# Performance work log

Hardware: AMD Instinct MI355X
Metric: run time of the kernel (lower is better)

## Reference

```python
import jax, jax.numpy as jnp
import numpy as np

B, C, H, W = 8, 256, 32, 32
DK, HEADS = 64, 4
DQ = DK * HEADS            # lambda attention: query dim = dim_key * num_heads
DV = 256 // HEADS          # out_channels // num_heads
EPS = 1e-5
SF = DK ** (-0.25)


def setup_inputs() -> dict:
    key = jax.random.key(0)
    ks = jax.random.split(key, 6)
    inv = 1.0 / np.sqrt(C)
    return {
        "input": jax.random.normal(ks[0], (B, C, H, W), jnp.float32),
        "Wq": jax.random.normal(ks[1], (DQ, C), jnp.float32) * inv,
        "gamma_q": jnp.ones((DQ,), jnp.float32),
        "beta_q": jnp.zeros((DQ,), jnp.float32),
        "Wk": jax.random.normal(ks[2], (DK, C), jnp.float32) * inv,
        "gamma_k": jnp.ones((DK,), jnp.float32),
        "beta_k": jnp.zeros((DK,), jnp.float32),
        "Wv": jax.random.normal(ks[3], (DV, C), jnp.float32) * inv,
        "rpe": jax.random.normal(ks[4], (2 * max(H, W) - 1, 2 * max(H, W) - 1, DK), jnp.float32),
    }


def _bn(x, gamma, beta):
    # BatchNorm2d in training mode: batch stats over (B, H, W), biased variance
    mu = jnp.mean(x, axis=(0, 2, 3), keepdims=True)
    var = jnp.var(x, axis=(0, 2, 3), keepdims=True)
    xn = (x - mu) * jax.lax.rsqrt(var + EPS)
    return xn * gamma[None, :, None, None] + beta[None, :, None, None]


def reference(input, Wq, gamma_q, beta_q, Wk, gamma_k, beta_k, Wv, rpe):
    b, c, h, w = input.shape
    n = h * w
    size = max(h, w)

    # conv1x1 projections (no bias)
    q = _bn(jnp.einsum('oc,bchw->bohw', Wq, input), gamma_q, beta_q)
    k = _bn(jnp.einsum('oc,bchw->bohw', Wk, input), gamma_k, beta_k)
    v = jnp.einsum('oc,bchw->bohw', Wv, input)

    q = q.reshape(b, HEADS, DK, n) * SF          # [b,h,k,n]
    k = k.reshape(b, DK, n) * SF                 # single kv head -> [b,k,n]
    v = v.reshape(b, DV, n)                      # [b,v,n]

    # lambda attention: content lambda
    ks = jax.nn.softmax(k, axis=-1)
    context = jnp.einsum('bkn,bvn->bkv', ks, v)
    out = jnp.einsum('bkv,bhkn->bhvn', context, q)

    # positional lambda via relative position embedding gather
    pos = jnp.arange(size)
    grid = jnp.stack(jnp.meshgrid(pos, pos, indexing='ij'), axis=-1).reshape(-1, 2)  # [n,2]
    rel = grid[None, :] - grid[:, None] + (size - 1)                                 # [n,n,2]
    rg = rpe[rel[..., 0], rel[..., 1]]                                               # [n,n,k]
    pos_context = jnp.einsum('nmk,bvm->bnkv', rg, v)
    out = out + jnp.einsum('bhkn,bnkv->bhvn', q, pos_context)

    return out.reshape(b, -1, h, w)
```

## Files before the change

### kernel.cpp

```cpp
#include <hip/hip_runtime.h>

#define SFC 0.35355339059327373f

typedef __attribute__((ext_vector_type(8))) short short8;
typedef __attribute__((ext_vector_type(16))) float f32x16;
typedef unsigned short ushort_t;

__device__ __forceinline__ float4 ld4(const float* p) { return *reinterpret_cast<const float4*>(p); }
__device__ __forceinline__ void st4(float* p, float4 v) { *reinterpret_cast<float4*>(p) = v; }

union F4 { float4 v; float f[4]; };
union S8 { short8 v; ushort_t u[8]; };

__device__ __forceinline__ ushort_t bfb(float f) {
  union { float f; unsigned u; } a; a.f = f;
  unsigned r = a.u + 0x7FFFu + ((a.u >> 16) & 1u);
  return (ushort_t)(r >> 16);
}

__device__ __forceinline__ void gl16(const void* g, void* l) {
  __builtin_amdgcn_global_load_lds(
      (const __attribute__((address_space(1))) unsigned int*)g,
      (__attribute__((address_space(3))) unsigned int*)l, 16, 0, 0);
}

__global__ __launch_bounds__(256) void k_prep(
    const float* __restrict__ rpe, const float* __restrict__ wq,
    const float* __restrict__ wk, const float* __restrict__ wv,
    const float* __restrict__ x, ushort_t* __restrict__ RPEB,
    ushort_t* __restrict__ WB, ushort_t* __restrict__ XBT)
{
  const int bx = blockIdx.x, t = threadIdx.x;
  if (bx < 63) {
    const int di = bx;
#pragma unroll
    for (int i = 0; i < 2; ++i) {
      const int c = t + i * 256;
      if (c < 504) {
        const int dj = c >> 3, k8 = (c & 7) * 8;
        const float* s = rpe + (size_t)di * 4032 + dj * 64 + k8;
        float4 a = ld4(s), b = ld4(s + 4);
        S8 o;
        o.u[0] = bfb(a.x); o.u[1] = bfb(a.y); o.u[2] = bfb(a.z); o.u[3] = bfb(a.w);
        o.u[4] = bfb(b.x); o.u[5] = bfb(b.y); o.u[6] = bfb(b.z); o.u[7] = bfb(b.w);
        *(short8*)(RPEB + (size_t)di * 4608 + dj * 72 + k8) = o.v;
      }
    }
  } else if (bx < 111) {
    const int cc = (bx - 63) * 256 + t;
    const int o = cc >> 5, k8 = (cc & 31) * 8;
    const float* src = (o < 256) ? (wq + o * 256)
                      : (o < 320) ? (wk + (o - 256) * 256)
                                  : (wv + (o - 320) * 256);
    float4 a = ld4(src + k8), b = ld4(src + k8 + 4);
    S8 s;
    s.u[0] = bfb(a.x); s.u[1] = bfb(a.y); s.u[2] = bfb(a.z); s.u[3] = bfb(a.w);
    s.u[4] = bfb(b.x); s.u[5] = bfb(b.y); s.u[6] = bfb(b.z); s.u[7] = bfb(b.w);
    *(short8*)(WB + (size_t)o * 256 + k8) = s.v;
  } else {
    const int id = (bx - 111) * 256 + t;
    const int ng = id & 8191, c8 = id >> 13;
    const int bb = ng >> 10, nn = ng & 1023;
    const float* src = x + (size_t)bb * 262144 + (size_t)(c8 * 8) * 1024 + nn;
    S8 s;
#pragma unroll
    for (int j = 0; j < 8; ++j) s.u[j] = bfb(src[(size_t)j * 1024]);
    *(short8*)(XBT + (size_t)ng * 256 + c8 * 8) = s.v;
  }
}

__global__ __launch_bounds__(256) void k_projm(
    const ushort_t* __restrict__ WB, const ushort_t* __restrict__ XBT,
    float* __restrict__ P, ushort_t* __restrict__ VB)
{
  __shared__ ushort_t At[64 * 72];
  __shared__ ushort_t Bt[128 * 72];
  const int t = threadIdx.x;
  const int bm = blockIdx.x, bn = blockIdx.y;
  const int o0 = bm * 64, col0 = bn * 128;
  const int w = t >> 6, l = t & 63, ln = l & 31, hi = l >> 5;
  const int wm = w & 1, wn = w >> 1;

  f32x16 acc0, acc1;
#pragma unroll
  for (int i = 0; i < 16; ++i) { acc0[i] = 0.f; acc1[i] = 0.f; }

  for (int k0 = 0; k0 < 256; k0 += 64) {
    __syncthreads();
#pragma unroll
    for (int i = 0; i < 2; ++i) {
      const int c = t + i * 256, row = c >> 3, k8 = (c & 7) * 8;
      *(short8*)(At + row * 72 + k8) =
          *(const short8*)(WB + (size_t)(o0 + row) * 256 + k0 + k8);
    }
#pragma unroll
    for (int i = 0; i < 4; ++i) {
      const int c = t + i * 256, row = c >> 3, k8 = (c & 7) * 8;
      *(short8*)(Bt + row * 72 + k8) =
          *(const short8*)(XBT + (size_t)(col0 + row) * 256 + k0 + k8);
    }
    __syncthreads();
    const ushort_t* ka  = At + (wm * 32 + ln) * 72 + hi * 8;
    const ushort_t* kb0 = Bt + (wn * 64 + ln) * 72 + hi * 8;
    const ushort_t* kb1 = Bt + (wn * 64 + 32 + ln) * 72 + hi * 8;
#pragma unroll
    for (int kc = 0; kc < 4; ++kc) {
      short8 a = *(const short8*)(ka + kc * 16);
      acc0 = __builtin_amdgcn_mfma_f32_32x32x16_bf16(a, *(const short8*)(kb0 + kc * 16), acc0, 0, 0, 0);
      acc1 = __builtin_amdgcn_mfma_f32_32x32x16_bf16(a, *(const short8*)(kb1 + kc * 16), acc1, 0, 0, 0);
    }
  }

#pragma unroll
  for (int r = 0; r < 16; ++r) {
    const int o = o0 + wm * 32 + (r & 3) + 8 * (r >> 2) + 4 * hi;
    float* dst = P + (size_t)o * 8192 + col0 + wn * 64 + ln;
    dst[0]  = acc0[r];
    dst[32] = acc1[r];
  }
  if (bm == 5) {
    const int b2 = bn >> 3;
#pragma unroll
    for (int r = 0; r < 16; ++r) {
      const int v = wm * 32 + (r & 3) + 8 * (r >> 2) + 4 * hi;
      const int i20 = (bn & 7) * 4 + wn * 2;
      VB[(size_t)(b2 * 32 + i20) * 2560 + v * 40 + ln]     = bfb(acc0[r]);
      VB[(size_t)(b2 * 32 + i20 + 1) * 2560 + v * 40 + ln] = bfb(acc1[r]);
    }
  }
}

__global__ __launch_bounds__(256) void k_stats(
    const float* __restrict__ P, const float* __restrict__ gq,
    const float* __restrict__ bq, const float* __restrict__ gk,
    const float* __restrict__ bk, float* __restrict__ scale,
    float* __restrict__ shift)
{
  const int ch = blockIdx.x;
  const float4* row = (const float4*)(P + (size_t)ch * 8192);
  float s = 0.f, ss = 0.f;
  for (int i = threadIdx.x; i < 2048; i += 256) {
    float4 v = row[i];
    s  += v.x + v.y + v.z + v.w;
    ss += v.x * v.x + v.y * v.y + v.z * v.z + v.w * v.w;
  }
#pragma unroll
  for (int off = 32; off; off >>= 1) {
    s  += __shfl_down(s, off, 64);
    ss += __shfl_down(ss, off, 64);
  }
  __shared__ float red[8];
  const int w = threadIdx.x >> 6, lane = threadIdx.x & 63;
  if (lane == 0) { red[w] = s; red[4 + w] = ss; }
  __syncthreads();
  if (threadIdx.x == 0) {
    s = red[0] + red[1] + red[2] + red[3];
    ss = red[4] + red[5] + red[6] + red[7];
    const float mu = s * (1.0f / 8192.0f);
    const float var = ss * (1.0f / 8192.0f) - mu * mu;
    const float rsig = rsqrtf(var + 1e-5f);
    float g, be;
    if (ch < 256) { g = gq[ch]; be = bq[ch]; }
    else          { g = gk[ch - 256]; be = bk[ch - 256]; }
    const float sc = rsig * g * SFC;
    scale[ch] = sc;
    shift[ch] = be * SFC - mu * sc;
  }
}

__global__ __launch_bounds__(256) void k_softmax(
    const float* __restrict__ P, const float* __restrict__ scale,
    const float* __restrict__ shift, float* __restrict__ KS)
{
  const int b = blockIdx.x >> 6, kc = blockIdx.x & 63;
  const int ch = 256 + kc;
  const float4* row = (const float4*)(P + (size_t)ch * 8192 + b * 1024);
  const float sc = scale[ch], sh = shift[ch];
  float4 v = row[threadIdx.x];
  float y0 = v.x * sc + sh, y1 = v.y * sc + sh;
  float y2 = v.z * sc + sh, y3 = v.w * sc + sh;
  float m = fmaxf(fmaxf(y0, y1), fmaxf(y2, y3));
#pragma unroll
  for (int off = 32; off; off >>= 1) m = fmaxf(m, __shfl_xor(m, off, 64));
  __shared__ float red[8];
  const int w = threadIdx.x >> 6, lane = threadIdx.x & 63;
  if (lane == 0) red[w] = m;
  __syncthreads();
  m = fmaxf(fmaxf(red[0], red[1]), fmaxf(red[2], red[3]));
  const float e0 = __expf(y0 - m), e1 = __expf(y1 - m);
  const float e2 = __expf(y2 - m), e3 = __expf(y3 - m);
  float su = e0 + e1 + e2 + e3;
#pragma unroll
  for (int off = 32; off; off >>= 1) su += __shfl_xor(su, off, 64);
  if (lane == 0) red[4 + w] = su;
  __syncthreads();
  const float inv = 1.0f / (red[4] + red[5] + red[6] + red[7]);
  ((float4*)(KS + (size_t)(b * 64 + kc) * 1024))[threadIdx.x] =
      make_float4(e0 * inv, e1 * inv, e2 * inv, e3 * inv);
}

__global__ __launch_bounds__(256) void k_ctx(
    const float* __restrict__ KS, const float* __restrict__ P,
    float* __restrict__ ctxp)
{
  __shared__ float ksl[64][64];
  __shared__ float vl[64][64];
  const int t = threadIdx.x;
  const int b = blockIdx.x;
  const int n0 = blockIdx.y * 64;
  {
    const int c = t >> 2, q4 = (t & 3) * 16;
    const float* s = KS + (size_t)(b * 64 + c) * 1024 + n0 + q4;
#pragma unroll
    for (int i = 0; i < 16; ++i) ksl[q4 + i][c] = s[i];
    const float* v = P + (size_t)(320 + c) * 8192 + b * 1024 + n0 + q4;
#pragma unroll
    for (int i = 0; i < 16; ++i) vl[q4 + i][c] = v[i];
  }
  __syncthreads();
  const int tr = t >> 4, tc = t & 15;
  float acc[4][4] = {};
#pragma unroll 4
  for (int nn = 0; nn < 64; ++nn) {
    F4 a; a.v = ld4(&ksl[nn][tr * 4]);
    F4 bv; bv.v = ld4(&vl[nn][tc * 4]);
#pragma unroll
    for (int i = 0; i < 4; ++i)
#pragma unroll
      for (int j = 0; j < 4; ++j) acc[i][j] += a.f[i] * bv.f[j];
  }
  float* dst = ctxp + (size_t)(b * 16 + blockIdx.y) * 4096;
#pragma unroll
  for (int i = 0; i < 4; ++i)
    st4(dst + (tr * 4 + i) * 64 + tc * 4,
        make_float4(acc[i][0], acc[i][1], acc[i][2], acc[i][3]));
}

__global__ __launch_bounds__(256) void k_ctxred(
    const float* __restrict__ ctxp, ushort_t* __restrict__ ctxb)
{
  const int i = blockIdx.x * 256 + threadIdx.x;
  const int b = i >> 12, r = i & 4095, kc = r >> 6, vc = r & 63;
  float s = 0.f;
#pragma unroll
  for (int c = 0; c < 16; ++c) s += ctxp[(size_t)(b * 16 + c) * 4096 + r];
  ctxb[(size_t)b * 4608 + vc * 72 + kc] = bfb(s);
}

extern __shared__ char ldsc[];

__global__ __launch_bounds__(512) void k_pos(
    const float* __restrict__ P, const ushort_t* __restrict__ RPEB,
    const ushort_t* __restrict__ VB, const float* __restrict__ scale,
    const float* __restrict__ shift, const ushort_t* __restrict__ CTXB,
    float* __restrict__ out)
{
  float* qst = (float*)ldsc;
  char* RbC = ldsc + 33792;
  char* VbC = ldsc + 70656;
  ushort_t* SlB = (ushort_t*)(ldsc + 91136);

  const int t = threadIdx.x;
  const int b = blockIdx.x >> 5, i1 = blockIdx.x & 31;
  const int w = t >> 6, l = t & 63, ln = l & 31, hi = l >> 5;
  const int m = w & 3, g = w >> 2;

  auto stage = [&](int i2, int buf) {
    const char* rs = (const char*)RPEB + (size_t)(i2 - i1 + 31) * 9216;
    const char* vs = (const char*)VB + (size_t)(b * 32 + i2) * 5120;
    char* rd = RbC + g * 18432 + buf * 9216;
    char* vd = VbC + g * 10240 + buf * 5120;
#pragma unroll
    for (int j = 0; j < 4; ++j) {
      const int chunk = m * 4 + j;
      const int off = chunk * 1024 + l * 16;
      if (chunk < 9)       gl16(rs + off, rd + off);
      else if (chunk < 14) gl16(vs + off - 9216, vd + off - 9216);
    }
  };

  const int i2base = g * 16;
  stage(i2base, 0);

  {
    const int j1 = t & 31, c0 = (t >> 5) * 16;
    const float* src = P + (size_t)b * 1024 + i1 * 32 + j1;
#pragma unroll
    for (int i = 0; i < 16; ++i) {
      const int ch = c0 + i;
      qst[ch * 33 + j1] = src[(size_t)ch * 8192] * scale[ch] + shift[ch];
    }
  }
  __syncthreads();

  short8 qf[4];
#pragma unroll
  for (int kc = 0; kc < 4; ++kc) {
    S8 s;
#pragma unroll
    for (int i = 0; i < 8; ++i)
      s.u[i] = bfb(qst[(m * 64 + kc * 16 + hi * 8 + i) * 33 + ln]);
    qf[kc] = s.v;
  }

  f32x16 sv0, sv1;
#pragma unroll
  for (int i = 0; i < 16; ++i) { sv0[i] = 0.f; sv1[i] = 0.f; }

  ushort_t* sm = SlB + w * 1280;

  for (int s = 0; s < 16; ++s) {
    const int cur = s & 1;
    if (s + 1 < 16) stage(i2base + s + 1, cur ^ 1);

    f32x16 t0, t1;
#pragma unroll
    for (int i = 0; i < 16; ++i) { t0[i] = 0.f; t1[i] = 0.f; }
    {
      const ushort_t* rb = (const ushort_t*)(RbC + g * 18432 + cur * 9216);
      const ushort_t* r0 = rb + ln * 72 + hi * 8;
      const ushort_t* r1 = rb + (32 + ln) * 72 + hi * 8;
#pragma unroll
      for (int kc = 0; kc < 4; ++kc) {
        t0 = __builtin_amdgcn_mfma_f32_32x32x16_bf16(qf[kc], *(const short8*)(r0 + kc * 16), t0, 0, 0, 0);
        t1 = __builtin_amdgcn_mfma_f32_32x32x16_bf16(qf[kc], *(const short8*)(r1 + kc * 16), t1, 0, 0, 0);
      }
    }
#pragma unroll
    for (int r = 0; r < 16; ++r) {
      const int j1 = (r & 3) + 8 * (r >> 2) + 4 * hi;
      const int j2a = ln + j1 - 31;
      const int j2b = 32 + ln + j1 - 31;
      if ((unsigned)j2a < 32u) sm[j1 * 40 + j2a] = bfb(t0[r]);
      if ((unsigned)j2b < 32u) sm[j1 * 40 + j2b] = bfb(t1[r]);
    }
    {
      const ushort_t* sa = sm + ln * 40 + hi * 8;
      const ushort_t* vbp = (const ushort_t*)(VbC + g * 10240 + cur * 5120);
      const ushort_t* v0 = vbp + ln * 40 + hi * 8;
      const ushort_t* v1 = vbp + (32 + ln) * 40 + hi * 8;
      short8 sA0 = *(const short8*)(sa);
      short8 sA1 = *(const short8*)(sa + 16);
      sv0 = __builtin_amdgcn_mfma_f32_32x32x16_bf16(sA0, *(const short8*)(v0),      sv0, 0, 0, 0);
      sv0 = __builtin_amdgcn_mfma_f32_32x32x16_bf16(sA1, *(const short8*)(v0 + 16), sv0, 0, 0, 0);
      sv1 = __builtin_amdgcn_mfma_f32_32x32x16_bf16(sA0, *(const short8*)(v1),      sv1, 0, 0, 0);
      sv1 = __builtin_amdgcn_mfma_f32_32x32x16_bf16(sA1, *(const short8*)(v1 + 16), sv1, 0, 0, 0);
    }
    __syncthreads();
  }

  {
    const char* cs = (const char*)CTXB + (size_t)b * 9216;
    gl16(cs + w * 1024 + l * 16, RbC + w * 1024 + l * 16);
    if (w == 0) gl16(cs + 8192 + l * 16, RbC + 8192 + l * 16);
  }
  __syncthreads();

  float* out_l = qst;
  if (g == 0) {
    const ushort_t* cb = (const ushort_t*)RbC;
    const ushort_t* c0 = cb + ln * 72 + hi * 8;
    const ushort_t* c1 = cb + (32 + ln) * 72 + hi * 8;
#pragma unroll
    for (int kc = 0; kc < 4; ++kc) {
      sv0 = __builtin_amdgcn_mfma_f32_32x32x16_bf16(qf[kc], *(const short8*)(c0 + kc * 16), sv0, 0, 0, 0);
      sv1 = __builtin_amdgcn_mfma_f32_32x32x16_bf16(qf[kc], *(const short8*)(c1 + kc * 16), sv1, 0, 0, 0);
    }
  } else {
#pragma unroll
    for (int r = 0; r < 16; ++r) {
      const int j1 = (r & 3) + 8 * (r >> 2) + 4 * hi;
      out_l[(m * 64 + ln) * 33 + j1]      = sv0[r];
      out_l[(m * 64 + 32 + ln) * 33 + j1] = sv1[r];
    }
  }
  __syncthreads();
  if (g == 0) {
#pragma unroll
    for (int r = 0; r < 16; ++r) {
      const int j1 = (r & 3) + 8 * (r >> 2) + 4 * hi;
      out_l[(m * 64 + ln) * 33 + j1]      += sv0[r];
      out_l[(m * 64 + 32 + ln) * 33 + j1] += sv1[r];
    }
  }
  __syncthreads();
  {
    const int ch = t >> 1, jh = (t & 1) * 16;
    float* dst = out + (size_t)b * 262144 + (size_t)ch * 1024 + i1 * 32 + jh;
    const float* srow = out_l + ch * 33 + jh;
#pragma unroll
    for (int gq2 = 0; gq2 < 4; ++gq2)
      st4(dst + gq2 * 4, make_float4(srow[gq2 * 4], srow[gq2 * 4 + 1],
                                     srow[gq2 * 4 + 2], srow[gq2 * 4 + 3]));
  }
}

extern "C" void kernel_launch(void* const* d_in, const int* in_sizes, int n_in,
                              void* d_out, int out_size, void* d_ws, size_t ws_size,
                              hipStream_t stream) {
  const float* x   = (const float*)d_in[0];
  const float* wq  = (const float*)d_in[1];
  const float* gq  = (const float*)d_in[2];
  const float* bq  = (const float*)d_in[3];
  const float* wk  = (const float*)d_in[4];
  const float* gk  = (const float*)d_in[5];
  const float* bk  = (const float*)d_in[6];
  const float* wv  = (const float*)d_in[7];
  const float* rpe = (const float*)d_in[8];
  float* out = (float*)d_out;
  char* W = (char*)d_ws;

  float* P        = (float*)W;
  float* KS       = (float*)(W + 12582912);
  float* SCALE    = (float*)(W + 14680064);
  float* SHIFT    = (float*)(W + 14681344);
  float* CTXP     = (float*)(W + 14682624);
  ushort_t* CTXB  = (ushort_t*)(W + 16779776);
  ushort_t* RPEB  = (ushort_t*)(W + 16853504);
  ushort_t* VB    = (ushort_t*)(W + 17434112);
  ushort_t* WB    = (ushort_t*)(W + 18744832);
  ushort_t* XBT   = (ushort_t*)(W + 18941440);

  k_prep<<<1135, 256, 0, stream>>>(rpe, wq, wk, wv, x, RPEB, WB, XBT);
  k_projm<<<dim3(6, 64), 256, 0, stream>>>(WB, XBT, P, VB);
  k_stats<<<320, 256, 0, stream>>>(P, gq, bq, gk, bk, SCALE, SHIFT);
  k_softmax<<<512, 256, 0, stream>>>(P, SCALE, SHIFT, KS);
  k_ctx<<<dim3(8, 16), 256, 0, stream>>>(KS, P, CTXP);
  k_ctxred<<<128, 256, 0, stream>>>(CTXP, CTXB);

  hipFuncSetAttribute((const void*)k_pos,
                      hipFuncAttributeMaxDynamicSharedMemorySize, 111616);
  k_pos<<<256, 512, 111616, stream>>>(P, RPEB, VB, SCALE, SHIFT, CTXB, out);
}
```

Baseline: 64.69 us.

## Fuse BN stats into projection GEMM, MFMA context kernel, deeper k_pos pipeline

The separate BatchNorm stats pass is removed. The projection GEMM epilogue now reduces per-channel sum and sum-of-squares with shuffles and atomics, and consumers compute scale and shift inline. The context reduction is rewritten as a single bf16 MFMA kernel over all n, with softmax writing bf16, which replaces the fp32 partial-sum kernel and its separate reduction. k_pos moves from double buffering to a 4-slot buffer ring with prefetch distance 2, explicit vmcnt waits and setprio around the MFMAs. The cost is more LDS, float atomic nondeterminism, and k_ctxm running only 8 blocks.

```diff
diff --git a/kernel.cpp b/kernel.cpp
--- a/kernel.cpp
+++ b/kernel.cpp
@@ -28,11 +28,15 @@
     const float* __restrict__ rpe, const float* __restrict__ wq,
     const float* __restrict__ wk, const float* __restrict__ wv,
     const float* __restrict__ x, ushort_t* __restrict__ RPEB,
-    ushort_t* __restrict__ WB, ushort_t* __restrict__ XBT)
+    ushort_t* __restrict__ WB, ushort_t* __restrict__ XBT,
+    float* __restrict__ SUM, float* __restrict__ SUMSQ)
 {
   const int bx = blockIdx.x, t = threadIdx.x;
   if (bx < 63) {
     const int di = bx;
+    if (bx == 0) {
+      for (int i = t; i < 320; i += 256) { SUM[i] = 0.f; SUMSQ[i] = 0.f; }
+    }
 #pragma unroll
     for (int i = 0; i < 2; ++i) {
       const int c = t + i * 256;
@@ -71,7 +75,8 @@
 
 __global__ __launch_bounds__(256) void k_projm(
     const ushort_t* __restrict__ WB, const ushort_t* __restrict__ XBT,
-    float* __restrict__ P, ushort_t* __restrict__ VB)
+    float* __restrict__ P, ushort_t* __restrict__ VB,
+    float* __restrict__ SUM, float* __restrict__ SUMSQ)
 {
   __shared__ ushort_t At[64 * 72];
   __shared__ ushort_t Bt[128 * 72];
@@ -127,55 +132,38 @@
       VB[(size_t)(b2 * 32 + i20) * 2560 + v * 40 + ln]     = bfb(acc0[r]);
       VB[(size_t)(b2 * 32 + i20 + 1) * 2560 + v * 40 + ln] = bfb(acc1[r]);
     }
-  }
-}
-
-__global__ __launch_bounds__(256) void k_stats(
-    const float* __restrict__ P, const float* __restrict__ gq,
-    const float* __restrict__ bq, const float* __restrict__ gk,
-    const float* __restrict__ bk, float* __restrict__ scale,
-    float* __restrict__ shift)
-{
-  const int ch = blockIdx.x;
-  const float4* row = (const float4*)(P + (size_t)ch * 8192);
-  float s = 0.f, ss = 0.f;
-  for (int i = threadIdx.x; i < 2048; i += 256) {
-    float4 v = row[i];
-    s  += v.x + v.y + v.z + v.w;
-    ss += v.x * v.x + v.y * v.y + v.z * v.z + v.w * v.w;
-  }
-#pragma unroll
-  for (int off = 32; off; off >>= 1) {
-    s  += __shfl_down(s, off, 64);
-    ss += __shfl_down(ss, off, 64);
-  }
-  __shared__ float red[8];
-  const int w = threadIdx.x >> 6, lane = threadIdx.x & 63;
-  if (lane == 0) { red[w] = s; red[4 + w] = ss; }
-  __syncthreads();
-  if (threadIdx.x == 0) {
-    s = red[0] + red[1] + red[2] + red[3];
-    ss = red[4] + red[5] + red[6] + red[7];
-    const float mu = s * (1.0f / 8192.0f);
-    const float var = ss * (1.0f / 8192.0f) - mu * mu;
-    const float rsig = rsqrtf(var + 1e-5f);
-    float g, be;
-    if (ch < 256) { g = gq[ch]; be = bq[ch]; }
-    else          { g = gk[ch - 256]; be = bk[ch - 256]; }
-    const float sc = rsig * g * SFC;
-    scale[ch] = sc;
-    shift[ch] = be * SFC - mu * sc;
+  } else {
+#pragma unroll
+    for (int r = 0; r < 16; ++r) {
+      float s1 = acc0[r] + acc1[r];
+      float s2 = acc0[r] * acc0[r] + acc1[r] * acc1[r];
+#pragma unroll
+      for (int off = 1; off < 32; off <<= 1) {
+        s1 += __shfl_xor(s1, off, 64);
+        s2 += __shfl_xor(s2, off, 64);
+      }
+      if (ln == 0) {
+        const int o = o0 + wm * 32 + (r & 3) + 8 * (r >> 2) + 4 * hi;
+        atomicAdd(&SUM[o], s1);
+        atomicAdd(&SUMSQ[o], s2);
+      }
+    }
   }
 }
 
 __global__ __launch_bounds__(256) void k_softmax(
-    const float* __restrict__ P, const float* __restrict__ scale,
-    const float* __restrict__ shift, float* __restrict__ KS)
+    const float* __restrict__ P, const float* __restrict__ SUM,
+    const float* __restrict__ SUMSQ, const float* __restrict__ gk,
+    const float* __restrict__ bk, ushort_t* __restrict__ KSB)
 {
   const int b = blockIdx.x >> 6, kc = blockIdx.x & 63;
   const int ch = 256 + kc;
+  const float mu = SUM[ch] * (1.0f / 8192.0f);
+  const float var = SUMSQ[ch] * (1.0f / 8192.0f) - mu * mu;
+  const float sc0 = rsqrtf(var + 1e-5f) * gk[kc] * SFC;
+  const float sc = sc0, sh = bk[kc] * SFC - mu * sc0;
+
   const float4* row = (const float4*)(P + (size_t)ch * 8192 + b * 1024);
-  const float sc = scale[ch], sh = shift[ch];
   float4 v = row[threadIdx.x];
   float y0 = v.x * sc + sh, y1 = v.y * sc + sh;
   float y2 = v.z * sc + sh, y3 = v.w * sc + sh;
@@ -195,92 +183,100 @@
   if (lane == 0) red[4 + w] = su;
   __syncthreads();
   const float inv = 1.0f / (red[4] + red[5] + red[6] + red[7]);
-  ((float4*)(KS + (size_t)(b * 64 + kc) * 1024))[threadIdx.x] =
-      make_float4(e0 * inv, e1 * inv, e2 * inv, e3 * inv);
-}
-
-__global__ __launch_bounds__(256) void k_ctx(
-    const float* __restrict__ KS, const float* __restrict__ P,
-    float* __restrict__ ctxp)
+  ushort4 u;
+  u.x = bfb(e0 * inv); u.y = bfb(e1 * inv);
+  u.z = bfb(e2 * inv); u.w = bfb(e3 * inv);
+  ((ushort4*)(KSB + (size_t)(b * 64 + kc) * 1024))[threadIdx.x] = u;
+}
+
+__global__ __launch_bounds__(256) void k_ctxm(
+    const ushort_t* __restrict__ KSB, const ushort_t* __restrict__ VB,
+    ushort_t* __restrict__ CTXB)
 {
-  __shared__ float ksl[64][64];
-  __shared__ float vl[64][64];
-  const int t = threadIdx.x;
-  const int b = blockIdx.x;
-  const int n0 = blockIdx.y * 64;
-  {
-    const int c = t >> 2, q4 = (t & 3) * 16;
-    const float* s = KS + (size_t)(b * 64 + c) * 1024 + n0 + q4;
-#pragma unroll
-    for (int i = 0; i < 16; ++i) ksl[q4 + i][c] = s[i];
-    const float* v = P + (size_t)(320 + c) * 8192 + b * 1024 + n0 + q4;
-#pragma unroll
-    for (int i = 0; i < 16; ++i) vl[q4 + i][c] = v[i];
-  }
-  __syncthreads();
-  const int tr = t >> 4, tc = t & 15;
-  float acc[4][4] = {};
-#pragma unroll 4
-  for (int nn = 0; nn < 64; ++nn) {
-    F4 a; a.v = ld4(&ksl[nn][tr * 4]);
-    F4 bv; bv.v = ld4(&vl[nn][tc * 4]);
-#pragma unroll
-    for (int i = 0; i < 4; ++i)
-#pragma unroll
-      for (int j = 0; j < 4; ++j) acc[i][j] += a.f[i] * bv.f[j];
-  }
-  float* dst = ctxp + (size_t)(b * 16 + blockIdx.y) * 4096;
-#pragma unroll
-  for (int i = 0; i < 4; ++i)
-    st4(dst + (tr * 4 + i) * 64 + tc * 4,
-        make_float4(acc[i][0], acc[i][1], acc[i][2], acc[i][3]));
-}
-
-__global__ __launch_bounds__(256) void k_ctxred(
-    const float* __restrict__ ctxp, ushort_t* __restrict__ ctxb)
-{
-  const int i = blockIdx.x * 256 + threadIdx.x;
-  const int b = i >> 12, r = i & 4095, kc = r >> 6, vc = r & 63;
-  float s = 0.f;
-#pragma unroll
-  for (int c = 0; c < 16; ++c) s += ctxp[(size_t)(b * 16 + c) * 4096 + r];
-  ctxb[(size_t)b * 4608 + vc * 72 + kc] = bfb(s);
+  __shared__ ushort_t KT[2][64 * 72];
+  __shared__ ushort_t VT[2][64 * 72];
+  const int b = blockIdx.x, t = threadIdx.x;
+  const int w = t >> 6, l = t & 63, ln = l & 31, hi = l >> 5;
+  const int a = w & 1, bt = w >> 1;
+
+  auto stageC = [&](int ch, int buf) {
+    const int n0 = ch * 64;
+#pragma unroll
+    for (int it = 0; it < 2; ++it) {
+      const int idx = t + it * 256;
+      const int row = idx >> 3, seg = idx & 7;
+      *(short8*)(&KT[buf][row * 72 + seg * 8]) =
+          *(const short8*)(KSB + (size_t)(b * 64 + row) * 1024 + n0 + seg * 8);
+      const int i2h = (n0 >> 5) + (seg >> 2);
+      *(short8*)(&VT[buf][row * 72 + seg * 8]) =
+          *(const short8*)(VB + (size_t)(b * 32 + i2h) * 2560 + row * 40 + (seg & 3) * 8);
+    }
+  };
+
+  f32x16 acc;
+#pragma unroll
+  for (int i = 0; i < 16; ++i) acc[i] = 0.f;
+
+  stageC(0, 0);
+  for (int ch = 0; ch < 16; ++ch) {
+    const int cur = ch & 1;
+    __syncthreads();
+    if (ch + 1 < 16) stageC(ch + 1, cur ^ 1);
+    const ushort_t* ka = &KT[cur][(a * 32 + ln) * 72 + hi * 8];
+    const ushort_t* kb = &VT[cur][(bt * 32 + ln) * 72 + hi * 8];
+#pragma unroll
+    for (int kc = 0; kc < 4; ++kc)
+      acc = __builtin_amdgcn_mfma_f32_32x32x16_bf16(
+          *(const short8*)(ka + kc * 16), *(const short8*)(kb + kc * 16), acc, 0, 0, 0);
+  }
+#pragma unroll
+  for (int r = 0; r < 16; ++r) {
+    const int kc = a * 32 + (r & 3) + 8 * (r >> 2) + 4 * hi;
+    CTXB[(size_t)b * 4608 + (bt * 32 + ln) * 72 + kc] = bfb(acc[r]);
+  }
 }
 
 extern __shared__ char ldsc[];
 
 __global__ __launch_bounds__(512) void k_pos(
     const float* __restrict__ P, const ushort_t* __restrict__ RPEB,
-    const ushort_t* __restrict__ VB, const float* __restrict__ scale,
-    const float* __restrict__ shift, const ushort_t* __restrict__ CTXB,
+    const ushort_t* __restrict__ VB, const float* __restrict__ SUM,
+    const float* __restrict__ SUMSQ, const float* __restrict__ gq,
+    const float* __restrict__ bq, const ushort_t* __restrict__ CTXB,
     float* __restrict__ out)
 {
   float* qst = (float*)ldsc;
-  char* RbC = ldsc + 33792;
-  char* VbC = ldsc + 70656;
-  ushort_t* SlB = (ushort_t*)(ldsc + 91136);
+  ushort_t* SlB = (ushort_t*)(ldsc + 119808);
 
   const int t = threadIdx.x;
   const int b = blockIdx.x >> 5, i1 = blockIdx.x & 31;
   const int w = t >> 6, l = t & 63, ln = l & 31, hi = l >> 5;
   const int m = w & 3, g = w >> 2;
 
+  auto bufp = [&](int buf, int gg) -> char* {
+    char* base = (buf < 3) ? (ldsc + 33792 + buf * 28672) : ldsc;
+    return base + gg * 14336;
+  };
+
   auto stage = [&](int i2, int buf) {
     const char* rs = (const char*)RPEB + (size_t)(i2 - i1 + 31) * 9216;
     const char* vs = (const char*)VB + (size_t)(b * 32 + i2) * 5120;
-    char* rd = RbC + g * 18432 + buf * 9216;
-    char* vd = VbC + g * 10240 + buf * 5120;
+    char* bb_ = bufp(buf, g);
+    char* rd = bb_;
+    char* vd = bb_ + 9216;
+    const int off = l * 16;
 #pragma unroll
     for (int j = 0; j < 4; ++j) {
-      const int chunk = m * 4 + j;
-      const int off = chunk * 1024 + l * 16;
-      if (chunk < 9)       gl16(rs + off, rd + off);
-      else if (chunk < 14) gl16(vs + off - 9216, vd + off - 9216);
+      const int c = m * 4 + j;
+      if (c < 9)       gl16(rs + c * 1024 + off, rd + c * 1024 + off);
+      else if (c < 14) gl16(vs + (c - 9) * 1024 + off, vd + (c - 9) * 1024 + off);
+      else             gl16(rs + (c - 14) * 1024 + off, rd + (c - 14) * 1024 + off);
     }
   };
 
   const int i2base = g * 16;
-  stage(i2base, 0);
+  stage(i2base + 0, 0);
+  stage(i2base + 1, 1);
 
   {
     const int j1 = t & 31, c0 = (t >> 5) * 16;
@@ -288,7 +284,11 @@
 #pragma unroll
     for (int i = 0; i < 16; ++i) {
       const int ch = c0 + i;
-      qst[ch * 33 + j1] = src[(size_t)ch * 8192] * scale[ch] + shift[ch];
+      const float mu = SUM[ch] * (1.0f / 8192.0f);
+      const float var = SUMSQ[ch] * (1.0f / 8192.0f) - mu * mu;
+      const float sc = rsqrtf(var + 1e-5f) * gq[ch] * SFC;
+      const float sh = bq[ch] * SFC - mu * sc;
+      qst[ch * 33 + j1] = src[(size_t)ch * 8192] * sc + sh;
     }
   }
   __syncthreads();
@@ -302,6 +302,7 @@
       s.u[i] = bfb(qst[(m * 64 + kc * 16 + hi * 8 + i) * 33 + ln]);
     qf[kc] = s.v;
   }
+  __syncthreads();
 
   f32x16 sv0, sv1;
 #pragma unroll
@@ -310,21 +311,29 @@
   ushort_t* sm = SlB + w * 1280;
 
   for (int s = 0; s < 16; ++s) {
-    const int cur = s & 1;
-    if (s + 1 < 16) stage(i2base + s + 1, cur ^ 1);
-
+    const int cur = s & 3;
+    if (s + 2 < 16) stage(i2base + s + 2, (s + 2) & 3);
+    if (s < 14)       asm volatile("s_waitcnt vmcnt(8)" ::: "memory");
+    else if (s == 14) asm volatile("s_waitcnt vmcnt(4)" ::: "memory");
+    else              asm volatile("s_waitcnt vmcnt(0)" ::: "memory");
+    __builtin_amdgcn_sched_barrier(0);
+    __builtin_amdgcn_s_barrier();
+
+    const char* bb_ = bufp(cur, g);
     f32x16 t0, t1;
 #pragma unroll
     for (int i = 0; i < 16; ++i) { t0[i] = 0.f; t1[i] = 0.f; }
     {
-      const ushort_t* rb = (const ushort_t*)(RbC + g * 18432 + cur * 9216);
+      const ushort_t* rb = (const ushort_t*)bb_;
       const ushort_t* r0 = rb + ln * 72 + hi * 8;
       const ushort_t* r1 = rb + (32 + ln) * 72 + hi * 8;
+      __builtin_amdgcn_s_setprio(1);
 #pragma unroll
       for (int kc = 0; kc < 4; ++kc) {
         t0 = __builtin_amdgcn_mfma_f32_32x32x16_bf16(qf[kc], *(const short8*)(r0 + kc * 16), t0, 0, 0, 0);
         t1 = __builtin_amdgcn_mfma_f32_32x32x16_bf16(qf[kc], *(const short8*)(r1 + kc * 16), t1, 0, 0, 0);
       }
+      __builtin_amdgcn_s_setprio(0);
     }
 #pragma unroll
     for (int r = 0; r < 16; ++r) {
@@ -336,29 +345,31 @@
     }
     {
       const ushort_t* sa = sm + ln * 40 + hi * 8;
-      const ushort_t* vbp = (const ushort_t*)(VbC + g * 10240 + cur * 5120);
+      const ushort_t* vbp = (const ushort_t*)(bb_ + 9216);
       const ushort_t* v0 = vbp + ln * 40 + hi * 8;
       const ushort_t* v1 = vbp + (32 + ln) * 40 + hi * 8;
       short8 sA0 = *(const short8*)(sa);
       short8 sA1 = *(const short8*)(sa + 16);
+      __builtin_amdgcn_s_setprio(1);
       sv0 = __builtin_amdgcn_mfma_f32_32x32x16_bf16(sA0, *(const short8*)(v0),      sv0, 0, 0, 0);
       sv0 = __builtin_amdgcn_mfma_f32_32x32x16_bf16(sA1, *(const short8*)(v0 + 16), sv0, 0, 0, 0);
       sv1 = __builtin_amdgcn_mfma_f32_32x32x16_bf16(sA0, *(const short8*)(v1),      sv1, 0, 0, 0);
       sv1 = __builtin_amdgcn_mfma_f32_32x32x16_bf16(sA1, *(const short8*)(v1 + 16), sv1, 0, 0, 0);
-    }
-    __syncthreads();
+      __builtin_amdgcn_s_setprio(0);
+    }
   }
 
   {
+    char* cdst = bufp(0, 0);
     const char* cs = (const char*)CTXB + (size_t)b * 9216;
-    gl16(cs + w * 1024 + l * 16, RbC + w * 1024 + l * 16);
-    if (w == 0) gl16(cs + 8192 + l * 16, RbC + 8192 + l * 16);
+    if (w < 8) gl16(cs + w * 1024 + l * 16, cdst + w * 1024 + l * 16);
+    if (w == 0) gl16(cs + 8192 + l * 16, cdst + 8192 + l * 16);
   }
   __syncthreads();
 
   float* out_l = qst;
   if (g == 0) {
-    const ushort_t* cb = (const ushort_t*)RbC;
+    const ushort_t* cb = (const ushort_t*)bufp(0, 0);
     const ushort_t* c0 = cb + ln * 72 + hi * 8;
     const ushort_t* c1 = cb + (32 + ln) * 72 + hi * 8;
 #pragma unroll
@@ -389,9 +400,9 @@
     float* dst = out + (size_t)b * 262144 + (size_t)ch * 1024 + i1 * 32 + jh;
     const float* srow = out_l + ch * 33 + jh;
 #pragma unroll
-    for (int gq2 = 0; gq2 < 4; ++gq2)
-      st4(dst + gq2 * 4, make_float4(srow[gq2 * 4], srow[gq2 * 4 + 1],
-                                     srow[gq2 * 4 + 2], srow[gq2 * 4 + 3]));
+    for (int gg = 0; gg < 4; ++gg)
+      st4(dst + gg * 4, make_float4(srow[gg * 4], srow[gg * 4 + 1],
+                                    srow[gg * 4 + 2], srow[gg * 4 + 3]));
   }
 }
 
@@ -411,24 +422,21 @@
   char* W = (char*)d_ws;
 
   float* P        = (float*)W;
-  float* KS       = (float*)(W + 12582912);
-  float* SCALE    = (float*)(W + 14680064);
-  float* SHIFT    = (float*)(W + 14681344);
-  float* CTXP     = (float*)(W + 14682624);
-  ushort_t* CTXB  = (ushort_t*)(W + 16779776);
-  ushort_t* RPEB  = (ushort_t*)(W + 16853504);
-  ushort_t* VB    = (ushort_t*)(W + 17434112);
-  ushort_t* WB    = (ushort_t*)(W + 18744832);
-  ushort_t* XBT   = (ushort_t*)(W + 18941440);
-
-  k_prep<<<1135, 256, 0, stream>>>(rpe, wq, wk, wv, x, RPEB, WB, XBT);
-  k_projm<<<dim3(6, 64), 256, 0, stream>>>(WB, XBT, P, VB);
-  k_stats<<<320, 256, 0, stream>>>(P, gq, bq, gk, bk, SCALE, SHIFT);
-  k_softmax<<<512, 256, 0, stream>>>(P, SCALE, SHIFT, KS);
-  k_ctx<<<dim3(8, 16), 256, 0, stream>>>(KS, P, CTXP);
-  k_ctxred<<<128, 256, 0, stream>>>(CTXP, CTXB);
+  ushort_t* KSB   = (ushort_t*)(W + 12582912);
+  float* SUM      = (float*)(W + 13631488);
+  float* SUMSQ    = (float*)(W + 13633536);
+  ushort_t* CTXB  = (ushort_t*)(W + 13635584);
+  ushort_t* RPEB  = (ushort_t*)(W + 13709312);
+  ushort_t* VB    = (ushort_t*)(W + 14289920);
+  ushort_t* WB    = (ushort_t*)(W + 15600640);
+  ushort_t* XBT   = (ushort_t*)(W + 15797248);
+
+  k_prep<<<1135, 256, 0, stream>>>(rpe, wq, wk, wv, x, RPEB, WB, XBT, SUM, SUMSQ);
+  k_projm<<<dim3(6, 64), 256, 0, stream>>>(WB, XBT, P, VB, SUM, SUMSQ);
+  k_softmax<<<512, 256, 0, stream>>>(P, SUM, SUMSQ, gk, bk, KSB);
+  k_ctxm<<<8, 256, 0, stream>>>(KSB, VB, CTXB);
 
   hipFuncSetAttribute((const void*)k_pos,
-                      hipFuncAttributeMaxDynamicSharedMemorySize, 111616);
-  k_pos<<<256, 512, 111616, stream>>>(P, RPEB, VB, SCALE, SHIFT, CTXB, out);
-}
+                      hipFuncAttributeMaxDynamicSharedMemorySize, 140288);
+  k_pos<<<256, 512, 140288, stream>>>(P, RPEB, VB, SUM, SUMSQ, gq, bq, CTXB, out);
+}
```

Result: slower. 88.25 us (+36.4%).
